# Kernel optimization log

Hardware: AMD Instinct MI355X
Metric: run time of the kernel (lower is better)

Reference implementation:

```python
import jax, jax.numpy as jnp
import numpy as np

N_USERS = 50000
N_ENTITIES = 100000
D = 64
R = 16
E_UI = 1500000
E_KG = 100000


def setup_inputs() -> dict:
    key = jax.random.key(0)
    ks = jax.random.split(key, 7)
    s = 1.0 / np.sqrt(D)  # ~xavier scale
    return {
        "user_indices": jnp.arange(N_USERS, dtype=jnp.int32),
        "item_indices": jnp.arange(N_ENTITIES, dtype=jnp.int32),
        "edge_index_ui": jax.random.randint(ks[0], (2, E_UI), 0, N_USERS + N_ENTITIES, dtype=jnp.int32),
        "edge_index_kg": jax.random.randint(ks[1], (2, E_KG), 0, N_ENTITIES, dtype=jnp.int32),
        "edge_type_kg": jax.random.randint(ks[2], (E_KG,), 0, R, dtype=jnp.int32),
        "user_table": (jax.random.normal(ks[3], (N_USERS, D)) * s).astype(jnp.float32),
        "entity_table": (jax.random.normal(ks[4], (N_ENTITIES, D)) * s).astype(jnp.float32),
        "W": (jax.random.normal(ks[5], (D, D)) * s).astype(jnp.float32),
        "W_r": (jax.random.normal(ks[6], (R, D, D)) * s).astype(jnp.float32),
    }


def _kgat_layer(x, edge_index, W, W_r, edge_type=None):
    # PyG aggr='add', flow source_to_target: x_j = x[src], x_i = x[dst], scatter to dst
    src, dst = edge_index[0], edge_index[1]
    x_j = x[src]  # [E, D]
    x_i = x[dst]  # [E, D]
    if edge_type is None:
        x_j_t = x_j @ W  # [E, D]
    else:
        # per-edge relation-specific transform: bmm(x_j[:,None,:], W_r[edge_type])
        x_j_t = jnp.einsum('ed,edo->eo', x_j, W_r[edge_type])
    # bi-interaction attention
    x_i_t = x_i @ W
    logits = jnp.sum(x_i_t * x_j_t, axis=1, keepdims=True)  # [E, 1]
    logits = jax.nn.leaky_relu(logits, negative_slope=0.2)
    scores = jax.nn.softmax(logits, axis=0)  # GLOBAL softmax over all edges (as in source)
    msg = scores * x_j_t  # [E, D]
    return jax.ops.segment_sum(msg, dst, num_segments=x.shape[0])


def reference(user_indices, item_indices, edge_index_ui, edge_index_kg, edge_type_kg,
              user_table, entity_table, W, W_r):
    user_embeds = user_table[user_indices]      # [n_users, D]
    item_embeds = entity_table[item_indices]    # [n_entities, D]
    x = jnp.concatenate([user_embeds, item_embeds], axis=0)
    # single layer (layer_dims = [embed_dim])
    x_ui = _kgat_layer(x, edge_index_ui, W, W_r, edge_type=None)
    x_kg = _kgat_layer(item_embeds, edge_index_kg, W, W_r, edge_type=edge_type_kg)
    x = x.at[N_USERS:].add(x_kg)  # faithful to source: overwritten by next line (dead store)
    x = jax.nn.relu(x_ui)
    # F.dropout(training=False) -> identity in eval mode
    return (x[:N_USERS], x[N_USERS:])
```

## Files before the change

kernel.cpp:

```cpp
#include <hip/hip_runtime.h>

#define NU 50000
#define NE 100000
#define NN 150000
#define DD 64
#define EUI 1500000
#define SPLIT 75008

#define TPB 256
#define NBLK 2048
#define NXB 2344
#define NXH (NXB + NBLK)
#define NBFA 4688
#define NBFB 4687
#define NHF (NBFA + NBLK)
#define NBF2 9375
#define NSC 9375

#define XWB_OFF    0ull
#define CNT_OFF    4800000ull
#define SCAL_OFF   4950000ull
#define PSUM_OFF   4950004ull
#define XWQ_OFF    4959424ull

__device__ __forceinline__ unsigned bfpack(float a, float b) {
  unsigned ua = __float_as_uint(a);
  ua = (ua + 0x7fffu + ((ua >> 16) & 1u)) >> 16;
  unsigned ub = __float_as_uint(b);
  ub = (ub + 0x7fffu + ((ub >> 16) & 1u)) & 0xffff0000u;
  return (ua & 0xffffu) | ub;
}

__device__ __forceinline__ unsigned q7pack4(float a, float b, float c, float d) {
  const float m = fmaxf(fmaxf(fabsf(a), fabsf(b)), fmaxf(fabsf(c), fabsf(d)));
  int E = -20;
  if (m >= 3.0517578125e-05f) {
    E = (int)((__float_as_uint(m) >> 23) & 0xffu) - 132;
    E = max(-20, min(-5, E));
  }
  const float s = __uint_as_float((unsigned)(127 - E) << 23);
  const int qa = max(-64, min(63, (int)rintf(a * s)));
  const int qb = max(-64, min(63, (int)rintf(b * s)));
  const int qc = max(-64, min(63, (int)rintf(c * s)));
  const int qd = max(-64, min(63, (int)rintf(d * s)));
  return ((unsigned)(E + 20) << 28) |
         (unsigned)(qa & 0x7f) | ((unsigned)(qb & 0x7f) << 7) |
         ((unsigned)(qc & 0x7f) << 14) | ((unsigned)(qd & 0x7f) << 21);
}

__device__ __forceinline__ void q7unpack4(unsigned v, float& s, float& a,
                                          float& b, float& c, float& d) {
  s = __uint_as_float(((v >> 28) + 107u) << 23);
  a = (float)((int)(v << 25) >> 25);
  b = (float)((int)(v << 18) >> 25);
  c = (float)((int)(v << 11) >> 25);
  d = (float)((int)(v << 4) >> 25);
}

template <int CTRL>
__device__ __forceinline__ float dpp_add(float x) {
  int y = __builtin_amdgcn_update_dpp(0, __float_as_int(x), CTRL, 0xF, 0xF, false);
  return x + __int_as_float(y);
}
__device__ __forceinline__ float row16_sum(float x) {
  x = dpp_add<0x124>(x);
  x = dpp_add<0x128>(x);
  x = dpp_add<0xB1>(x);
  x = dpp_add<0x4E>(x);
  return x;
}

__device__ __forceinline__ void hist_body(int idx, const int* __restrict__ ei,
                                          unsigned* __restrict__ cnt,
                                          int* __restrict__ ssrcp,
                                          int lo, int hi) {
  for (int e = idx * TPB + threadIdx.x; e < EUI; e += NBLK * TPB) {
    const int dst = ei[EUI + e];
    if (dst < lo || dst >= hi) continue;
    const int src = ei[e];
    const unsigned r = atomicAdd(&cnt[dst], 1u);
    if (r < 64u) ssrcp[((size_t)dst << 6) + r] = src;
  }
}

__device__ __forceinline__ void fused_tile(int tile,
                                           const unsigned* __restrict__ cnt,
                                           const int* ssrcp,
                                           const unsigned* __restrict__ xwb,
                                           const unsigned* __restrict__ xwq,
                                           float* out,
                                           float* __restrict__ psum) {
  const int lane = threadIdx.x & 63;
  const int wv = threadIdx.x >> 6;
  const int sub = lane >> 4;
  const int q = lane & 15;
  const int n = tile * 16 + wv * 4 + sub;
  const uint2* __restrict__ x2 = (const uint2*)xwb;
  const uint2 dv = x2[(size_t)n * 16 + q];
  const float vd0 = __uint_as_float(dv.x << 16);
  const float vd1 = __uint_as_float(dv.x & 0xffff0000u);
  const float vd2 = __uint_as_float(dv.y << 16);
  const float vd3 = __uint_as_float(dv.y & 0xffff0000u);
  const int deg = min((int)cnt[n], 64);
  int dmax = deg;
  dmax = max(dmax, __shfl_xor(dmax, 16, 64));
  dmax = max(dmax, __shfl_xor(dmax, 32, 64));
  const size_t base = (size_t)n << 6;
  const int nit = (dmax + 3) >> 2;
  float a0 = 0.f, a1 = 0.f, a2 = 0.f, a3 = 0.f, wacc = 0.f;
  int4 sl = *(const int4*)(ssrcp + base);
  for (int ii = 0; ii < nit; ++ii) {
    const int it = 4 * ii;
    int s0 = sl.x, s1 = sl.y, s2 = sl.z, s3 = sl.w;
    if (ii + 1 < nit) sl = *(const int4*)(ssrcp + base + it + 4);
    const bool act0 = it < deg;
    const bool act1 = it + 1 < deg;
    const bool act2 = it + 2 < deg;
    const bool act3 = it + 3 < deg;
    if (!act0) s0 = 0;
    if (!act1) s1 = 0;
    if (!act2) s2 = 0;
    if (!act3) s3 = 0;
    const unsigned sv0 = xwq[(size_t)s0 * 16 + q];
    const unsigned sv1 = xwq[(size_t)s1 * 16 + q];
    const unsigned sv2 = xwq[(size_t)s2 * 16 + q];
    const unsigned sv3 = xwq[(size_t)s3 * 16 + q];
    float se0, u0, u1, u2, u3;
    float se1, t0, t1, t2, t3;
    float se2, g0, g1, g2, g3;
    float se3, h0, h1, h2, h3;
    q7unpack4(sv0, se0, u0, u1, u2, u3);
    q7unpack4(sv1, se1, t0, t1, t2, t3);
    q7unpack4(sv2, se2, g0, g1, g2, g3);
    q7unpack4(sv3, se3, h0, h1, h2, h3);
    float p0 = vd0 * u0;
    p0 = fmaf(vd1, u1, p0); p0 = fmaf(vd2, u2, p0); p0 = fmaf(vd3, u3, p0);
    float p1 = vd0 * t0;
    p1 = fmaf(vd1, t1, p1); p1 = fmaf(vd2, t2, p1); p1 = fmaf(vd3, t3, p1);
    float p2 = vd0 * g0;
    p2 = fmaf(vd1, g1, p2); p2 = fmaf(vd2, g2, p2); p2 = fmaf(vd3, g3, p2);
    float p3 = vd0 * h0;
    p3 = fmaf(vd1, h1, p3); p3 = fmaf(vd2, h2, p3); p3 = fmaf(vd3, h3, p3);
    p0 *= se0;
    p1 *= se1;
    p2 *= se2;
    p3 *= se3;
    p0 = row16_sum(p0);
    p1 = row16_sum(p1);
    p2 = row16_sum(p2);
    p3 = row16_sum(p3);
    const float l0 = (p0 > 0.f) ? p0 : 0.2f * p0;
    const float l1 = (p1 > 0.f) ? p1 : 0.2f * p1;
    const float l2 = (p2 > 0.f) ? p2 : 0.2f * p2;
    const float l3 = (p3 > 0.f) ? p3 : 0.2f * p3;
    float w0 = __expf(l0);
    float w1 = __expf(l1);
    float w2 = __expf(l2);
    float w3 = __expf(l3);
    if (!act0) w0 = 0.f;
    if (!act1) w1 = 0.f;
    if (!act2) w2 = 0.f;
    if (!act3) w3 = 0.f;
    const float ws0 = w0 * se0;
    const float ws1 = w1 * se1;
    const float ws2 = w2 * se2;
    const float ws3 = w3 * se3;
    a0 = fmaf(ws0, u0, a0); a1 = fmaf(ws0, u1, a1);
    a2 = fmaf(ws0, u2, a2); a3 = fmaf(ws0, u3, a3);
    a0 = fmaf(ws1, t0, a0); a1 = fmaf(ws1, t1, a1);
    a2 = fmaf(ws1, t2, a2); a3 = fmaf(ws1, t3, a3);
    a0 = fmaf(ws2, g0, a0); a1 = fmaf(ws2, g1, a1);
    a2 = fmaf(ws2, g2, a2); a3 = fmaf(ws2, g3, a3);
    a0 = fmaf(ws3, h0, a0); a1 = fmaf(ws3, h1, a1);
    a2 = fmaf(ws3, h2, a2); a3 = fmaf(ws3, h3, a3);
    wacc += (w0 + w1) + (w2 + w3);
  }
  float4 r = {a0, a1, a2, a3};
  ((float4*)(out + (size_t)n * DD))[q] = r;
  __shared__ float sm[16];
  if (q == 0) sm[wv * 4 + sub] = wacc;
  __syncthreads();
  if (threadIdx.x == 0) {
    float s = 0.f;
#pragma unroll
    for (int i = 0; i < 16; ++i) s += sm[i];
    psum[tile] = s;
  }
}

__global__ __launch_bounds__(TPB) void k_xw_histA(const int* __restrict__ uidx,
                                                  const int* __restrict__ iidx,
                                                  const float* __restrict__ ut,
                                                  const float* __restrict__ et,
                                                  const float* __restrict__ W,
                                                  unsigned* __restrict__ xwb,
                                                  unsigned* __restrict__ xwq,
                                                  const int* __restrict__ ei,
                                                  unsigned* __restrict__ cnt,
                                                  int* __restrict__ ssrcp) {
  const int bi = blockIdx.x;
  int idx;
  bool hist;
  if (bi < 2 * NBLK) { hist = (bi & 1); idx = bi >> 1; }
  else               { hist = false;    idx = bi - NBLK; }

  if (hist) {
    hist_body(idx, ei, cnt, ssrcp, 0, SPLIT);
    return;
  }

  __shared__ float Ws[DD * DD];
  __shared__ float Xs[64 * 68];
  const int t = threadIdx.x;
  {
    const float4* W4 = (const float4*)W;
    float4* Ws4 = (float4*)Ws;
#pragma unroll
    for (int i = 0; i < 4; ++i) Ws4[t + i * TPB] = W4[t + i * TPB];
  }
  {
    const int rl = t >> 2, ch = t & 3;
    int row = idx * 64 + rl;
    if (row >= NN) row = NN - 1;
    const float4* s4 = (const float4*)((row < NU)
        ? ut + (size_t)uidx[row] * DD
        : et + (size_t)iidx[row - NU] * DD);
    float4* x4 = (float4*)(Xs + rl * 68);
#pragma unroll
    for (int j = 0; j < 4; ++j) x4[ch + 4 * j] = s4[ch + 4 * j];
  }
  __syncthreads();
  const int q = t & 15, g = t >> 4;
  float4 acc[4] = {{0,0,0,0},{0,0,0,0},{0,0,0,0},{0,0,0,0}};
  const float* __restrict__ wsq = Ws + 4 * q;
  const float* __restrict__ xsg = Xs + (4 * g) * 68;
#pragma unroll 1
  for (int kc = 0; kc < 16; ++kc) {
    const float4 w0 = *(const float4*)(wsq + (4 * kc + 0) * DD);
    const float4 w1 = *(const float4*)(wsq + (4 * kc + 1) * DD);
    const float4 w2 = *(const float4*)(wsq + (4 * kc + 2) * DD);
    const float4 w3 = *(const float4*)(wsq + (4 * kc + 3) * DD);
#pragma unroll
    for (int i = 0; i < 4; ++i) {
      const float4 x = *(const float4*)(xsg + i * 68 + 4 * kc);
      acc[i].x = fmaf(x.x, w0.x, acc[i].x);
      acc[i].y = fmaf(x.x, w0.y, acc[i].y);
      acc[i].z = fmaf(x.x, w0.z, acc[i].z);
      acc[i].w = fmaf(x.x, w0.w, acc[i].w);
      acc[i].x = fmaf(x.y, w1.x, acc[i].x);
      acc[i].y = fmaf(x.y, w1.y, acc[i].y);
      acc[i].z = fmaf(x.y, w1.z, acc[i].z);
      acc[i].w = fmaf(x.y, w1.w, acc[i].w);
      acc[i].x = fmaf(x.z, w2.x, acc[i].x);
      acc[i].y = fmaf(x.z, w2.y, acc[i].y);
      acc[i].z = fmaf(x.z, w2.z, acc[i].z);
      acc[i].w = fmaf(x.z, w2.w, acc[i].w);
      acc[i].x = fmaf(x.w, w3.x, acc[i].x);
      acc[i].y = fmaf(x.w, w3.y, acc[i].y);
      acc[i].z = fmaf(x.w, w3.z, acc[i].z);
      acc[i].w = fmaf(x.w, w3.w, acc[i].w);
    }
  }
#pragma unroll
  for (int i = 0; i < 4; ++i) {
    const int row = idx * 64 + 4 * g + i;
    if (row < NN) {
      uint2 p;
      p.x = bfpack(acc[i].x, acc[i].y);
      p.y = bfpack(acc[i].z, acc[i].w);
      ((uint2*)(xwb + (size_t)row * 32))[q] = p;
      xwq[(size_t)row * 16 + q] = q7pack4(acc[i].x, acc[i].y, acc[i].z, acc[i].w);
    }
  }
}

__global__ __launch_bounds__(TPB) void k_histB_fusedA(const int* __restrict__ ei,
                                                      unsigned* __restrict__ cnt,
                                                      int* ssrcp,
                                                      const unsigned* __restrict__ xwb,
                                                      const unsigned* __restrict__ xwq,
                                                      float* out,
                                                      float* __restrict__ psum) {
  const int bi = blockIdx.x;
  int idx;
  bool hist;
  if (bi < 2 * NBLK) { hist = (bi & 1); idx = bi >> 1; }
  else               { hist = false;    idx = bi - NBLK; }

  if (hist) {
    hist_body(idx, ei, cnt, ssrcp, SPLIT, NN);
    return;
  }
  fused_tile(idx, cnt, ssrcp, xwb, xwq, out, psum);
}

__global__ __launch_bounds__(TPB) void k_fusedB(const unsigned* __restrict__ cnt,
                                                const int* ssrcp,
                                                const unsigned* __restrict__ xwb,
                                                const unsigned* __restrict__ xwq,
                                                float* out,
                                                float* __restrict__ psum) {
  fused_tile(NBFA + blockIdx.x, cnt, ssrcp, xwb, xwq, out, psum);
}

__global__ __launch_bounds__(TPB) void k_rsum(const float* __restrict__ psum,
                                              float* __restrict__ scal) {
  float s = 0.f;
  for (int i = threadIdx.x; i < NBF2; i += TPB) s += psum[i];
#pragma unroll
  for (int off = 32; off; off >>= 1) s += __shfl_xor(s, off, 64);
  __shared__ float sm[4];
  if ((threadIdx.x & 63) == 0) sm[threadIdx.x >> 6] = s;
  __syncthreads();
  if (threadIdx.x == 0) scal[0] = sm[0] + sm[1] + sm[2] + sm[3];
}

__global__ __launch_bounds__(TPB) void k_scale(float* __restrict__ out,
                                               const float* __restrict__ scal) {
  const float inv = 1.0f / scal[0];
  const int i = blockIdx.x * TPB + threadIdx.x;
  float4* o4 = (float4*)out;
  float4 v = o4[i];
  v.x = fmaxf(v.x * inv, 0.f);
  v.y = fmaxf(v.y * inv, 0.f);
  v.z = fmaxf(v.z * inv, 0.f);
  v.w = fmaxf(v.w * inv, 0.f);
  o4[i] = v;
}

extern "C" void kernel_launch(void* const* d_in, const int* in_sizes, int n_in,
                              void* d_out, int out_size, void* d_ws, size_t ws_size,
                              hipStream_t stream) {
  const int* uidx = (const int*)d_in[0];
  const int* iidx = (const int*)d_in[1];
  const int* ei_ui = (const int*)d_in[2];
  const float* ut = (const float*)d_in[5];
  const float* et = (const float*)d_in[6];
  const float* W = (const float*)d_in[7];

  float* out = (float*)d_out;
  float* ws = (float*)d_ws;
  unsigned* xwb = (unsigned*)(ws + XWB_OFF);
  unsigned* cnt = (unsigned*)(ws + CNT_OFF);
  float* scal = ws + SCAL_OFF;
  float* psum = ws + PSUM_OFF;
  unsigned* xwq = (unsigned*)(ws + XWQ_OFF);
  int* ssrcp = (int*)d_out;

  (void)hipMemsetAsync(cnt, 0, (size_t)NN * sizeof(unsigned), stream);

  k_xw_histA<<<NXH, TPB, 0, stream>>>(uidx, iidx, ut, et, W, xwb, xwq, ei_ui,
                                      cnt, ssrcp);
  k_histB_fusedA<<<NHF, TPB, 0, stream>>>(ei_ui, cnt, ssrcp, xwb, xwq, out, psum);
  k_fusedB<<<NBFB, TPB, 0, stream>>>(cnt, ssrcp, xwb, xwq, out, psum);
  k_rsum<<<1, TPB, 0, stream>>>(psum, scal);
  k_scale<<<NSC, TPB, 0, stream>>>(out, scal);
}
```

Baseline: 246.3 us.

## Split histogram/aggregation pipeline into three destination-range stages

The destination-sorted histogram pass is now split into three ranges (users, first and second halves of items) instead of two. Each stage's histogram runs interleaved with the fused aggregation tiles of the previous range, and a final kernel handles the last range's tiles. This aims to overlap more of the histogram work with gather/aggregation and to shrink the serialized tail, at the cost of one extra kernel launch and an extra pass over the edge list for histogramming.

```diff
diff --git a/kernel.cpp b/kernel.cpp
--- a/kernel.cpp
+++ b/kernel.cpp
@@ -5,15 +5,15 @@
 #define NN 150000
 #define DD 64
 #define EUI 1500000
-#define SPLIT 75008
+#define SP1 50000
+#define SP2 100000
 
 #define TPB 256
 #define NBLK 2048
 #define NXB 2344
 #define NXH (NXB + NBLK)
-#define NBFA 4688
-#define NBFB 4687
-#define NHF (NBFA + NBLK)
+#define NT1 3125
+#define NHF (NT1 + NBLK)
 #define NBF2 9375
 #define NSC 9375
 
@@ -188,7 +188,7 @@
   }
 }
 
-__global__ __launch_bounds__(TPB) void k_xw_histA(const int* __restrict__ uidx,
+__global__ __launch_bounds__(TPB) void k_xw_hist1(const int* __restrict__ uidx,
                                                   const int* __restrict__ iidx,
                                                   const float* __restrict__ ut,
                                                   const float* __restrict__ et,
@@ -205,7 +205,7 @@
   else               { hist = false;    idx = bi - NBLK; }
 
   if (hist) {
-    hist_body(idx, ei, cnt, ssrcp, 0, SPLIT);
+    hist_body(idx, ei, cnt, ssrcp, 0, SP1);
     return;
   }
 
@@ -274,33 +274,51 @@
   }
 }
 
-__global__ __launch_bounds__(TPB) void k_histB_fusedA(const int* __restrict__ ei,
-                                                      unsigned* __restrict__ cnt,
-                                                      int* ssrcp,
-                                                      const unsigned* __restrict__ xwb,
-                                                      const unsigned* __restrict__ xwq,
-                                                      float* out,
-                                                      float* __restrict__ psum) {
+__global__ __launch_bounds__(TPB) void k_h2_fA(const int* __restrict__ ei,
+                                               unsigned* __restrict__ cnt,
+                                               int* ssrcp,
+                                               const unsigned* __restrict__ xwb,
+                                               const unsigned* __restrict__ xwq,
+                                               float* out,
+                                               float* __restrict__ psum) {
   const int bi = blockIdx.x;
   int idx;
   bool hist;
   if (bi < 2 * NBLK) { hist = (bi & 1); idx = bi >> 1; }
   else               { hist = false;    idx = bi - NBLK; }
-
   if (hist) {
-    hist_body(idx, ei, cnt, ssrcp, SPLIT, NN);
+    hist_body(idx, ei, cnt, ssrcp, SP1, SP2);
     return;
   }
   fused_tile(idx, cnt, ssrcp, xwb, xwq, out, psum);
 }
 
-__global__ __launch_bounds__(TPB) void k_fusedB(const unsigned* __restrict__ cnt,
-                                                const int* ssrcp,
-                                                const unsigned* __restrict__ xwb,
-                                                const unsigned* __restrict__ xwq,
-                                                float* out,
-                                                float* __restrict__ psum) {
-  fused_tile(NBFA + blockIdx.x, cnt, ssrcp, xwb, xwq, out, psum);
+__global__ __launch_bounds__(TPB) void k_h3_fB(const int* __restrict__ ei,
+                                               unsigned* __restrict__ cnt,
+                                               int* ssrcp,
+                                               const unsigned* __restrict__ xwb,
+                                               const unsigned* __restrict__ xwq,
+                                               float* out,
+                                               float* __restrict__ psum) {
+  const int bi = blockIdx.x;
+  int idx;
+  bool hist;
+  if (bi < 2 * NBLK) { hist = (bi & 1); idx = bi >> 1; }
+  else               { hist = false;    idx = bi - NBLK; }
+  if (hist) {
+    hist_body(idx, ei, cnt, ssrcp, SP2, NN);
+    return;
+  }
+  fused_tile(NT1 + idx, cnt, ssrcp, xwb, xwq, out, psum);
+}
+
+__global__ __launch_bounds__(TPB) void k_fC(const unsigned* __restrict__ cnt,
+                                            const int* ssrcp,
+                                            const unsigned* __restrict__ xwb,
+                                            const unsigned* __restrict__ xwq,
+                                            float* out,
+                                            float* __restrict__ psum) {
+  fused_tile(2 * NT1 + blockIdx.x, cnt, ssrcp, xwb, xwq, out, psum);
 }
 
 __global__ __launch_bounds__(TPB) void k_rsum(const float* __restrict__ psum,
@@ -349,10 +367,11 @@
 
   (void)hipMemsetAsync(cnt, 0, (size_t)NN * sizeof(unsigned), stream);
 
-  k_xw_histA<<<NXH, TPB, 0, stream>>>(uidx, iidx, ut, et, W, xwb, xwq, ei_ui,
+  k_xw_hist1<<<NXH, TPB, 0, stream>>>(uidx, iidx, ut, et, W, xwb, xwq, ei_ui,
                                       cnt, ssrcp);
-  k_histB_fusedA<<<NHF, TPB, 0, stream>>>(ei_ui, cnt, ssrcp, xwb, xwq, out, psum);
-  k_fusedB<<<NBFB, TPB, 0, stream>>>(cnt, ssrcp, xwb, xwq, out, psum);
+  k_h2_fA<<<NHF, TPB, 0, stream>>>(ei_ui, cnt, ssrcp, xwb, xwq, out, psum);
+  k_h3_fB<<<NHF, TPB, 0, stream>>>(ei_ui, cnt, ssrcp, xwb, xwq, out, psum);
+  k_fC<<<NT1, TPB, 0, stream>>>(cnt, ssrcp, xwb, xwq, out, psum);
   k_rsum<<<1, TPB, 0, stream>>>(psum, scal);
   k_scale<<<NSC, TPB, 0, stream>>>(out, scal);
 }
```

Measured after the change: 256.7 us. 1.04x slower.
